# Optimization experiments

Measured on AMD Instinct MI355X. Metric: run time of the kernel, lower is better.

The kernel has to match this reference:

```python
import jax, jax.numpy as jnp
import numpy as np

EPS = 1e-5

def conv1x1(x, W, b):
    # x: [B,Cin,H,W], W: [Cout,Cin], b: [Cout]
    return jnp.einsum('bchw,oc->bohw', x, W) + b[None, :, None, None]

def mean_variance_norm(feat):
    # feat: [B,C,H,W]; torch .var(dim=2) is unbiased (ddof=1)
    B, C, H, W = feat.shape
    flat = feat.reshape(B, C, H * W)
    mean = flat.mean(axis=2)[:, :, None, None]
    std = jnp.sqrt(flat.var(axis=2, ddof=1) + EPS)[:, :, None, None]
    return (feat - mean) / std

def setup_inputs() -> dict:
    key = jax.random.key(0)
    ks = jax.random.split(key, 10)
    B, C, H, W = 4, 512, 64, 64
    sc = 0.02
    return {
        'content': jax.random.normal(ks[0], (B, C, H, W), jnp.float32),
        'style': jax.random.normal(ks[1], (B, C, H, W), jnp.float32),
        'content_key': jax.random.normal(ks[2], (B, C, H, W), jnp.float32),
        'style_key': jax.random.normal(ks[3], (B, C, H, W), jnp.float32),
        'Wf': jax.random.normal(ks[4], (C, C), jnp.float32) * sc,
        'bf': jax.random.normal(ks[5], (C,), jnp.float32) * sc,
        'Wg': jax.random.normal(ks[6], (C, C), jnp.float32) * sc,
        'bg': jax.random.normal(ks[7], (C,), jnp.float32) * sc,
        'Wh': jax.random.normal(ks[8], (C, C), jnp.float32) * sc,
        'bh': jax.random.normal(ks[9], (C,), jnp.float32) * sc,
    }

def reference(content, style, content_key, style_key, Wf, bf, Wg, bg, Wh, bh):
    B, C, H, W = content.shape
    F = conv1x1(content_key, Wf, bf)          # [B,Ck,H,W]
    G = conv1x1(style_key, Wg, bg)            # [B,Ck,Hs,Ws]
    Hv = conv1x1(style, Wh, bh)               # [B,C,Hs,Ws]
    Ck = F.shape[1]
    N = H * W
    M = G.shape[2] * G.shape[3]
    Fq = F.reshape(B, Ck, N).transpose(0, 2, 1)        # [B,N,Ck]
    Gk = G.reshape(B, Ck, M)                            # [B,Ck,M]
    style_flat = Hv.reshape(B, C, M).transpose(0, 2, 1)  # [B,M,C]
    S = jax.nn.softmax(jnp.einsum('bnc,bcm->bnm', Fq, Gk), axis=-1)  # [B,N,M]
    mean = jnp.einsum('bnm,bmc->bnc', S, style_flat)                  # [B,N,C]
    second = jnp.einsum('bnm,bmc->bnc', S, style_flat ** 2)
    std = jnp.sqrt(jax.nn.relu(second - mean ** 2))
    mean = mean.reshape(B, H, W, C).transpose(0, 3, 1, 2)
    std = std.reshape(B, H, W, C).transpose(0, 3, 1, 2)
    return std * mean_variance_norm(content) + mean
```

## Files before the change

kernel.cpp:

```cpp
#include <hip/hip_runtime.h>

#define B_ 4
#define C_ 512
#define N_ 4096

typedef unsigned short u16;
typedef _Float16 f16;
typedef f16 f16x8 __attribute__((ext_vector_type(8)));
typedef float f32x4 __attribute__((ext_vector_type(4)));

#define MFMA16(a, b, c) __builtin_amdgcn_mfma_f32_16x16x32_f16(a, b, c, 0, 0, 0)

__device__ __forceinline__ u16 f2h(float f) {
  union { f16 h; u16 u; } x; x.h = (f16)f; return x.u;
}
__device__ __forceinline__ float h2f(u16 v) {
  union { u16 u; f16 h; } x; x.u = v; return (float)x.h;
}
__device__ __forceinline__ f16x8 ldA(const void* p) {
  union { uint4 u; f16x8 v; } x; x.u = *(const uint4*)p; return x.v;
}

__global__ __launch_bounds__(256) void cast_w_kernel(const float* __restrict__ in,
                                                     u16* __restrict__ out, int n) {
  int i = (blockIdx.x * 256 + threadIdx.x) * 4;
  if (i >= n) return;
  float4 v = *(const float4*)(in + i);
  uint2 p;
  p.x = f2h(v.x) | ((unsigned)f2h(v.y) << 16);
  p.y = f2h(v.z) | ((unsigned)f2h(v.w) << 16);
  *(uint2*)(out + i) = p;
}

__global__ __launch_bounds__(256) void transpose_cast_kernel(const float* __restrict__ in,
                                                             u16* __restrict__ out) {
  __shared__ float ld[64][65];
  const int b = blockIdx.z, n0 = blockIdx.x * 64, c0 = blockIdx.y * 64;
  const int t = threadIdx.x;
  {
    const int r = t >> 2, q4 = (t & 3) * 16;
    const float* ip = in + ((size_t)(b * C_ + c0 + r)) * N_ + n0 + q4;
#pragma unroll
    for (int j = 0; j < 4; ++j) {
      float4 v = *(const float4*)(ip + j * 4);
      ld[r][q4 + j * 4 + 0] = v.x; ld[r][q4 + j * 4 + 1] = v.y;
      ld[r][q4 + j * 4 + 2] = v.z; ld[r][q4 + j * 4 + 3] = v.w;
    }
  }
  __syncthreads();
  {
    const int r2 = t >> 2, c16 = (t & 3) * 16;
    unsigned pk[8];
#pragma unroll
    for (int j = 0; j < 8; ++j) {
      unsigned lo = f2h(ld[c16 + j * 2 + 0][r2]);
      unsigned hi = f2h(ld[c16 + j * 2 + 1][r2]);
      pk[j] = lo | (hi << 16);
    }
    u16* op = out + ((size_t)(b * N_ + n0 + r2)) * C_ + c0 + c16;
    *(uint4*)(op + 0) = make_uint4(pk[0], pk[1], pk[2], pk[3]);
    *(uint4*)(op + 8) = make_uint4(pk[4], pk[5], pk[6], pk[7]);
  }
}

__global__ __launch_bounds__(512, 4) void conv_kernel(const u16* __restrict__ Xt,
                                                      const u16* __restrict__ Wb,
                                                      const float* __restrict__ bias,
                                                      u16* __restrict__ Outp,
                                                      u16* __restrict__ OutT) {
  __shared__ char sm[65536];
  const int b = blockIdx.z, n0 = blockIdx.x * 64, o0 = blockIdx.y * 64;
  const int t = threadIdx.x, w = t >> 6, lane = t & 63;
  const int wr = w >> 1, wc = w & 1, l15 = lane & 15, l4 = lane >> 4;
#pragma unroll
  for (int k = 0; k < 8; ++k) {
    int ch = t + k * 512, row = ch >> 6, c16 = ch & 63;
    uint4 xv = *(const uint4*)(Xt + ((size_t)(b * N_ + n0 + row)) * C_ + c16 * 8);
    *(uint4*)(sm + row * 1024 + ((c16 ^ (row & 7)) << 4)) = xv;
  }
  __syncthreads();
  f32x4 acc0 = {0, 0, 0, 0}, acc1 = {0, 0, 0, 0};
  const int arow = wr * 16 + l15;
  const int oA = o0 + wc * 32 + l15, oB = oA + 16;
  const u16* wp0 = Wb + (size_t)oA * C_ + l4 * 8;
  const u16* wp1 = Wb + (size_t)oB * C_ + l4 * 8;
#pragma unroll
  for (int kf = 0; kf < 16; ++kf) {
    f16x8 a = ldA(sm + arow * 1024 + (((kf * 4 + l4) ^ (arow & 7)) << 4));
    f16x8 w0 = ldA(wp0 + kf * 32);
    f16x8 w1 = ldA(wp1 + kf * 32);
    acc0 = MFMA16(a, w0, acc0);
    acc1 = MFMA16(a, w1, acc1);
  }
  const float b0 = bias[oA], b1 = bias[oB];
  if (OutT == nullptr) {
#pragma unroll
    for (int r = 0; r < 4; ++r) {
      int n = n0 + wr * 16 + l4 * 4 + r;
      size_t base = ((size_t)(b * N_ + n)) * C_;
      Outp[base + oA] = f2h(acc0[r] + b0);
      Outp[base + oB] = f2h(acc1[r] + b1);
    }
  } else {
    __syncthreads();
    u16* ldsT = (u16*)sm;
#pragma unroll
    for (int r = 0; r < 4; ++r) {
      int nl = wr * 16 + l4 * 4 + r;
      ldsT[(oA - o0) * 72 + nl] = f2h(acc0[r] + b0);
      ldsT[(oB - o0) * 72 + nl] = f2h(acc1[r] + b1);
    }
    __syncthreads();
    const int orow = t >> 3, n8 = (t & 7) * 8;
    uint4 v = *(const uint4*)&ldsT[orow * 72 + n8];
    *(uint4*)(OutT + ((size_t)(b * C_ + o0 + orow)) * N_ + n0 + n8) = v;
  }
}

#define LQ  0
#define LG  65536
#define LV  98304
#define LP  139264
#define LF  144384
#define LL  144640

__global__ __launch_bounds__(1024, 4) void attn_dual_kernel(const u16* __restrict__ Ft,
                                                            const u16* __restrict__ Gt,
                                                            const u16* __restrict__ V,
                                                            float* __restrict__ OutM,
                                                            float* __restrict__ OutS) {
  __shared__ char sm[144896];
  char* ldsQ = sm + LQ; char* ldsG = sm + LG; char* ldsV = sm + LV; char* ldsP = sm + LP;
  float* facv = (float*)(sm + LF);
  float* lbuf = (float*)(sm + LL);

  const int b = blockIdx.y, n0 = blockIdx.x * 64;
  const int t = threadIdx.x, w = t >> 6, lane = t & 63;
  const int l15 = lane & 15, l4 = lane >> 4;
  const int ri = w >> 2, ci = w & 3;

#pragma unroll
  for (int k = 0; k < 4; ++k) {
    int ch = t + k * 1024, row = ch >> 6, c16 = ch & 63;
    uint4 qv = *(const uint4*)(Ft + ((size_t)(b * N_ + n0 + row)) * C_ + c16 * 8);
    *(uint4*)(ldsQ + row * 1024 + ((c16 ^ (row & 7)) << 4)) = qv;
  }
#pragma unroll
  for (int k = 0; k < 2; ++k) {
    int ch = t + k * 1024, row = ch >> 6, c16 = ch & 63;
    uint4 gv = *(const uint4*)(Gt + ((size_t)(b * N_ + row)) * C_ + c16 * 8);
    *(uint4*)(ldsG + row * 1024 + ((c16 ^ (row & 7)) << 4)) = gv;
  }

  f32x4 accM[8], accS[8];
#pragma unroll
  for (int i = 0; i < 8; ++i) { accM[i] = (f32x4){0,0,0,0}; accS[i] = (f32x4){0,0,0,0}; }
  float m_run[4] = {-1e30f, -1e30f, -1e30f, -1e30f};
  float l_run[4] = {0, 0, 0, 0};

  const u16* Vb = V + (size_t)(b * C_) * N_;
  __syncthreads();

  for (int it = 0; it < 128; ++it) {
    const int m0 = it * 32;

    if (w < 4) {
      f32x4 s0 = {0, 0, 0, 0}, s1 = {0, 0, 0, 0};
      {
        const int qrow = w * 16 + l15;
        const int g0r = l15, g1r = 16 + l15;
#pragma unroll
        for (int kf = 0; kf < 16; ++kf) {
          int c16 = kf * 4 + l4;
          f16x8 qf = ldA(ldsQ + qrow * 1024 + ((c16 ^ (qrow & 7)) << 4));
          f16x8 ga = ldA(ldsG + g0r * 1024 + ((c16 ^ (g0r & 7)) << 4));
          f16x8 gb = ldA(ldsG + g1r * 1024 + ((c16 ^ (g1r & 7)) << 4));
          s0 = MFMA16(qf, ga, s0);
          s1 = MFMA16(qf, gb, s1);
        }
      }
      float rmax[4];
#pragma unroll
      for (int r = 0; r < 4; ++r) rmax[r] = fmaxf(s0[r], s1[r]);
#pragma unroll
      for (int off = 1; off < 16; off <<= 1)
#pragma unroll
        for (int r = 0; r < 4; ++r) rmax[r] = fmaxf(rmax[r], __shfl_xor(rmax[r], off));
      float fac0[4], rsum[4];
#pragma unroll
      for (int r = 0; r < 4; ++r) {
        float mn = fmaxf(m_run[r], rmax[r]);
        fac0[r] = __expf(m_run[r] - mn);
        float p0 = __expf(s0[r] - mn);
        float p1 = __expf(s1[r] - mn);
        u16 pb0 = f2h(p0), pb1 = f2h(p1);
        rsum[r] = h2f(pb0) + h2f(pb1);
        int row = w * 16 + l4 * 4 + r;
        *(u16*)(ldsP + row * 80 + l15 * 2) = pb0;
        *(u16*)(ldsP + row * 80 + 32 + l15 * 2) = pb1;
        m_run[r] = mn;
      }
#pragma unroll
      for (int off = 1; off < 16; off <<= 1)
#pragma unroll
        for (int r = 0; r < 4; ++r) rsum[r] += __shfl_xor(rsum[r], off);
      if (l15 == 0)
#pragma unroll
        for (int r = 0; r < 4; ++r) {
          int row = w * 16 + l4 * 4 + r;
          l_run[r] = l_run[r] * fac0[r] + rsum[r];
          facv[row] = fac0[r];
        }
      else
#pragma unroll
        for (int r = 0; r < 4; ++r) l_run[r] = l_run[r] * fac0[r] + rsum[r];
    } else if (w < 12) {
      const int t2 = t - 256;
#pragma unroll
      for (int k = 0; k < 4; ++k) {
        int ch = t2 + k * 512, c = ch >> 2, sl = ch & 3;
        uint4 vv = *(const uint4*)(Vb + (size_t)c * N_ + m0 + sl * 8);
        *(uint4*)(ldsV + c * 80 + sl * 16) = vv;
      }
    }
    __syncthreads();

    if (w >= 12 && it < 127) {
      const int t3 = t - 768;
      const u16* gb_ = Gt + ((size_t)(b * N_ + m0 + 32)) * C_;
#pragma unroll
      for (int k = 0; k < 8; ++k) {
        int ch = t3 + k * 256, row = ch >> 6, c16 = ch & 63;
        uint4 gv = *(const uint4*)(gb_ + (size_t)row * C_ + c16 * 8);
        *(uint4*)(ldsG + row * 1024 + ((c16 ^ (row & 7)) << 4)) = gv;
      }
    }
    float fr[4];
#pragma unroll
    for (int r = 0; r < 4; ++r) fr[r] = facv[ri * 16 + l4 * 4 + r];
    bool nch = true;
#pragma unroll
    for (int r = 0; r < 4; ++r) nch = nch && (fr[r] == 1.0f);
    if (!__all(nch)) {
#pragma unroll
      for (int f = 0; f < 8; ++f)
#pragma unroll
        for (int r = 0; r < 4; ++r) { accM[f][r] *= fr[r]; accS[f][r] *= fr[r]; }
    }
    {
      const int arow = ri * 16 + l15;
      f16x8 a = ldA(ldsP + arow * 80 + l4 * 16);
#pragma unroll
      for (int f = 0; f < 8; ++f) {
        const int c = ci * 128 + f * 16 + l15;
        f16x8 v0 = ldA(ldsV + c * 80 + l4 * 16);
        accM[f] = MFMA16(a, v0, accM[f]);
        f16x8 w0 = v0 * v0;
        accS[f] = MFMA16(a, w0, accS[f]);
      }
    }
    __syncthreads();
  }

  if (w < 4 && l15 == 0)
#pragma unroll
    for (int r = 0; r < 4; ++r) lbuf[w * 16 + l4 * 4 + r] = l_run[r];
  __syncthreads();
  float rl[4];
#pragma unroll
  for (int r = 0; r < 4; ++r) rl[r] = 1.0f / lbuf[ri * 16 + l4 * 4 + r];
#pragma unroll
  for (int f = 0; f < 8; ++f) {
    const int c = ci * 128 + f * 16 + l15;
#pragma unroll
    for (int r = 0; r < 4; ++r) {
      int n = n0 + ri * 16 + l4 * 4 + r;
      size_t o = ((size_t)(b * N_ + n)) * C_ + c;
      OutM[o] = accM[f][r] * rl[r];
      OutS[o] = accS[f][r] * rl[r];
    }
  }
}

__global__ __launch_bounds__(256) void stats_kernel(const float* __restrict__ content,
                                                    float* __restrict__ stats) {
  const int c = blockIdx.x, b = blockIdx.y;
  const float4* p = (const float4*)(content + ((size_t)(b * C_ + c)) * N_);
  float s = 0.f, ss = 0.f;
  for (int i = threadIdx.x; i < N_ / 4; i += 256) {
    float4 v = p[i];
    s += v.x + v.y + v.z + v.w;
    ss += v.x * v.x + v.y * v.y + v.z * v.z + v.w * v.w;
  }
#pragma unroll
  for (int off = 32; off; off >>= 1) { s += __shfl_down(s, off); ss += __shfl_down(ss, off); }
  __shared__ float as_[4], ass_[4];
  int w = threadIdx.x >> 6;
  if ((threadIdx.x & 63) == 0) { as_[w] = s; ass_[w] = ss; }
  __syncthreads();
  if (threadIdx.x == 0) {
    float S = as_[0] + as_[1] + as_[2] + as_[3];
    float SS = ass_[0] + ass_[1] + ass_[2] + ass_[3];
    float mu = S * (1.0f / N_);
    float var = (SS - (float)N_ * mu * mu) * (1.0f / (N_ - 1));
    stats[(size_t)(b * C_ + c) * 2 + 0] = mu;
    stats[(size_t)(b * C_ + c) * 2 + 1] = rsqrtf(var + 1e-5f);
  }
}

__global__ __launch_bounds__(256) void combine_kernel(const float* __restrict__ content,
                                                      const float* __restrict__ meanb,
                                                      const float* __restrict__ secb,
                                                      const float* __restrict__ stats,
                                                      float* __restrict__ outp) {
  __shared__ float ldM[64][65], ldS[64][65];
  const int b = blockIdx.z, n0 = blockIdx.x * 64, c0 = blockIdx.y * 64;
  const int t = threadIdx.x;
  {
    const int r = t >> 2, q4 = (t & 3) * 16;
    size_t ib = ((size_t)(b * N_ + n0 + r)) * C_ + c0 + q4;
#pragma unroll
    for (int j = 0; j < 4; ++j) {
      float4 mv = *(const float4*)(meanb + ib + j * 4);
      float4 sv = *(const float4*)(secb + ib + j * 4);
      ldM[r][q4 + j * 4 + 0] = mv.x; ldM[r][q4 + j * 4 + 1] = mv.y;
      ldM[r][q4 + j * 4 + 2] = mv.z; ldM[r][q4 + j * 4 + 3] = mv.w;
      ldS[r][q4 + j * 4 + 0] = sv.x; ldS[r][q4 + j * 4 + 1] = sv.y;
      ldS[r][q4 + j * 4 + 2] = sv.z; ldS[r][q4 + j * 4 + 3] = sv.w;
    }
  }
  __syncthreads();
  const int n4 = (t & 15) * 4, cb = t >> 4;
#pragma unroll
  for (int cc = 0; cc < 4; ++cc) {
    int c_loc = cc * 16 + cb;
    int c = c0 + c_loc;
    float mu = stats[(size_t)(b * C_ + c) * 2 + 0];
    float rs = stats[(size_t)(b * C_ + c) * 2 + 1];
    size_t gb = ((size_t)(b * C_ + c)) * N_ + n0 + n4;
    float4 xv = *(const float4*)(content + gb);
    float4 ov;
    {
      float m0_ = ldM[n4 + 0][c_loc], s0_ = ldS[n4 + 0][c_loc];
      float m1_ = ldM[n4 + 1][c_loc], s1_ = ldS[n4 + 1][c_loc];
      float m2_ = ldM[n4 + 2][c_loc], s2_ = ldS[n4 + 2][c_loc];
      float m3_ = ldM[n4 + 3][c_loc], s3_ = ldS[n4 + 3][c_loc];
      ov.x = sqrtf(fmaxf(s0_ - m0_ * m0_, 0.f)) * ((xv.x - mu) * rs) + m0_;
      ov.y = sqrtf(fmaxf(s1_ - m1_ * m1_, 0.f)) * ((xv.y - mu) * rs) + m1_;
      ov.z = sqrtf(fmaxf(s2_ - m2_ * m2_, 0.f)) * ((xv.z - mu) * rs) + m2_;
      ov.w = sqrtf(fmaxf(s3_ - m3_ * m3_, 0.f)) * ((xv.w - mu) * rs) + m3_;
    }
    *(float4*)(outp + gb) = ov;
  }
}

extern "C" void kernel_launch(void* const* d_in, const int* in_sizes, int n_in,
                              void* d_out, int out_size, void* d_ws, size_t ws_size,
                              hipStream_t stream) {
  (void)in_sizes; (void)n_in; (void)out_size; (void)ws_size;
  const float* content = (const float*)d_in[0];
  const float* style   = (const float*)d_in[1];
  const float* ckey    = (const float*)d_in[2];
  const float* skey    = (const float*)d_in[3];
  const float* Wf = (const float*)d_in[4]; const float* bf_ = (const float*)d_in[5];
  const float* Wg = (const float*)d_in[6]; const float* bg_ = (const float*)d_in[7];
  const float* Wh = (const float*)d_in[8]; const float* bh_ = (const float*)d_in[9];
  float* outp = (float*)d_out;
  char* ws = (char*)d_ws;

  const size_t MB = 1u << 20;
  u16*   Ft    = (u16*)(ws + 0 * MB);
  u16*   Gt    = (u16*)(ws + 16 * MB);
  u16*   Hv    = (u16*)(ws + 32 * MB);
  float* stats = (float*)(ws + 48 * MB);
  u16*   Xt    = (u16*)(ws + 48 * MB);
  float* meanb = (float*)(ws + 64 * MB);
  float* secb  = (float*)(ws + 96 * MB);
  u16*   Wb3   = (u16*)(ws + 80 * MB);
  u16* Wbf = Wb3, *Wbg = Wb3 + 262144, *Wbh = Wb3 + 524288;

  const dim3 gT(64, 8, 4);

  cast_w_kernel<<<256, 256, 0, stream>>>(Wf, Wbf, 262144);
  cast_w_kernel<<<256, 256, 0, stream>>>(Wg, Wbg, 262144);
  cast_w_kernel<<<256, 256, 0, stream>>>(Wh, Wbh, 262144);

  transpose_cast_kernel<<<gT, 256, 0, stream>>>(ckey, Xt);
  conv_kernel<<<gT, 512, 0, stream>>>(Xt, Wbf, bf_, Ft, nullptr);
  transpose_cast_kernel<<<gT, 256, 0, stream>>>(skey, Xt);
  conv_kernel<<<gT, 512, 0, stream>>>(Xt, Wbg, bg_, Gt, nullptr);
  transpose_cast_kernel<<<gT, 256, 0, stream>>>(style, Xt);
  conv_kernel<<<gT, 512, 0, stream>>>(Xt, Wbh, bh_, nullptr, Hv);

  stats_kernel<<<dim3(C_, B_), 256, 0, stream>>>(content, stats);
  attn_dual_kernel<<<dim3(64, B_), 1024, 0, stream>>>(Ft, Gt, Hv, meanb, secb);
  combine_kernel<<<gT, 256, 0, stream>>>(content, meanb, secb, stats, outp);
}
```

Measured before the change: 894.3 us.

## Fuse transpose-cast into 1x1 conv kernel, computing all output channels per block

Replaces the separate transpose/cast-to-fp16 pass plus conv kernel with one kernel that loads fp32 input tiles, transposes and casts them through LDS into a swizzled fp16 tile, then loops over all 512 output channels. This removes the intermediate Xt buffer round-trip through global memory and the extra launches per conv. The trade-off is a grid of only 256 blocks, each doing eight times the work serially with larger LDS use (about 80KB), which may lower occupancy and parallelism on a large GPU.

```diff
diff --git a/kernel.cpp b/kernel.cpp
--- a/kernel.cpp
+++ b/kernel.cpp
@@ -32,88 +32,84 @@
   *(uint2*)(out + i) = p;
 }
 
-__global__ __launch_bounds__(256) void transpose_cast_kernel(const float* __restrict__ in,
-                                                             u16* __restrict__ out) {
-  __shared__ float ld[64][65];
-  const int b = blockIdx.z, n0 = blockIdx.x * 64, c0 = blockIdx.y * 64;
-  const int t = threadIdx.x;
-  {
-    const int r = t >> 2, q4 = (t & 3) * 16;
-    const float* ip = in + ((size_t)(b * C_ + c0 + r)) * N_ + n0 + q4;
-#pragma unroll
-    for (int j = 0; j < 4; ++j) {
-      float4 v = *(const float4*)(ip + j * 4);
-      ld[r][q4 + j * 4 + 0] = v.x; ld[r][q4 + j * 4 + 1] = v.y;
-      ld[r][q4 + j * 4 + 2] = v.z; ld[r][q4 + j * 4 + 3] = v.w;
-    }
-  }
-  __syncthreads();
-  {
-    const int r2 = t >> 2, c16 = (t & 3) * 16;
-    unsigned pk[8];
-#pragma unroll
-    for (int j = 0; j < 8; ++j) {
-      unsigned lo = f2h(ld[c16 + j * 2 + 0][r2]);
-      unsigned hi = f2h(ld[c16 + j * 2 + 1][r2]);
-      pk[j] = lo | (hi << 16);
-    }
-    u16* op = out + ((size_t)(b * N_ + n0 + r2)) * C_ + c0 + c16;
-    *(uint4*)(op + 0) = make_uint4(pk[0], pk[1], pk[2], pk[3]);
-    *(uint4*)(op + 8) = make_uint4(pk[4], pk[5], pk[6], pk[7]);
-  }
-}
-
-__global__ __launch_bounds__(512, 4) void conv_kernel(const u16* __restrict__ Xt,
-                                                      const u16* __restrict__ Wb,
-                                                      const float* __restrict__ bias,
-                                                      u16* __restrict__ Outp,
-                                                      u16* __restrict__ OutT) {
-  __shared__ char sm[65536];
-  const int b = blockIdx.z, n0 = blockIdx.x * 64, o0 = blockIdx.y * 64;
+#define FCA 0
+#define FCB 65536
+
+__global__ __launch_bounds__(512, 4) void conv_fused_kernel(const float* __restrict__ X,
+                                                            const u16* __restrict__ Wb,
+                                                            const float* __restrict__ bias,
+                                                            u16* __restrict__ Outp,
+                                                            u16* __restrict__ OutT) {
+  __shared__ char sm[82176];
+  float* ld = (float*)(sm + FCB);
+  const int b = blockIdx.y, n0 = blockIdx.x * 64;
   const int t = threadIdx.x, w = t >> 6, lane = t & 63;
   const int wr = w >> 1, wc = w & 1, l15 = lane & 15, l4 = lane >> 4;
-#pragma unroll
-  for (int k = 0; k < 8; ++k) {
-    int ch = t + k * 512, row = ch >> 6, c16 = ch & 63;
-    uint4 xv = *(const uint4*)(Xt + ((size_t)(b * N_ + n0 + row)) * C_ + c16 * 8);
-    *(uint4*)(sm + row * 1024 + ((c16 ^ (row & 7)) << 4)) = xv;
-  }
-  __syncthreads();
-  f32x4 acc0 = {0, 0, 0, 0}, acc1 = {0, 0, 0, 0};
-  const int arow = wr * 16 + l15;
-  const int oA = o0 + wc * 32 + l15, oB = oA + 16;
-  const u16* wp0 = Wb + (size_t)oA * C_ + l4 * 8;
-  const u16* wp1 = Wb + (size_t)oB * C_ + l4 * 8;
-#pragma unroll
-  for (int kf = 0; kf < 16; ++kf) {
-    f16x8 a = ldA(sm + arow * 1024 + (((kf * 4 + l4) ^ (arow & 7)) << 4));
-    f16x8 w0 = ldA(wp0 + kf * 32);
-    f16x8 w1 = ldA(wp1 + kf * 32);
-    acc0 = MFMA16(a, w0, acc0);
-    acc1 = MFMA16(a, w1, acc1);
-  }
-  const float b0 = bias[oA], b1 = bias[oB];
-  if (OutT == nullptr) {
-#pragma unroll
-    for (int r = 0; r < 4; ++r) {
-      int n = n0 + wr * 16 + l4 * 4 + r;
-      size_t base = ((size_t)(b * N_ + n)) * C_;
-      Outp[base + oA] = f2h(acc0[r] + b0);
-      Outp[base + oB] = f2h(acc1[r] + b1);
-    }
-  } else {
+
+  for (int cc = 0; cc < 8; ++cc) {
+    {
+      const int r = t >> 3, q8 = (t & 7) * 8;
+      const float* ip = X + ((size_t)(b * C_ + cc * 64 + r)) * N_ + n0 + q8;
+      float4 v0 = *(const float4*)(ip);
+      float4 v1 = *(const float4*)(ip + 4);
+      float* lr = ld + r * 65 + q8;
+      lr[0] = v0.x; lr[1] = v0.y; lr[2] = v0.z; lr[3] = v0.w;
+      lr[4] = v1.x; lr[5] = v1.y; lr[6] = v1.z; lr[7] = v1.w;
+    }
     __syncthreads();
-    u16* ldsT = (u16*)sm;
-#pragma unroll
-    for (int r = 0; r < 4; ++r) {
-      int nl = wr * 16 + l4 * 4 + r;
-      ldsT[(oA - o0) * 72 + nl] = f2h(acc0[r] + b0);
-      ldsT[(oB - o0) * 72 + nl] = f2h(acc1[r] + b1);
+    {
+      const int r2 = t >> 3, c8 = (t & 7) * 8;
+      unsigned pk[4];
+#pragma unroll
+      for (int j = 0; j < 4; ++j) {
+        unsigned lo = f2h(ld[(c8 + j * 2 + 0) * 65 + r2]);
+        unsigned hi = f2h(ld[(c8 + j * 2 + 1) * 65 + r2]);
+        pk[j] = lo | (hi << 16);
+      }
+      const int c16 = cc * 8 + (t & 7);
+      *(uint4*)(sm + r2 * 1024 + ((c16 ^ (r2 & 7)) << 4)) =
+          make_uint4(pk[0], pk[1], pk[2], pk[3]);
     }
     __syncthreads();
-    const int orow = t >> 3, n8 = (t & 7) * 8;
-    uint4 v = *(const uint4*)&ldsT[orow * 72 + n8];
-    *(uint4*)(OutT + ((size_t)(b * C_ + o0 + orow)) * N_ + n0 + n8) = v;
+  }
+
+  for (int o0 = 0; o0 < 512; o0 += 64) {
+    f32x4 acc0 = {0, 0, 0, 0}, acc1 = {0, 0, 0, 0};
+    const int arow = wr * 16 + l15;
+    const int oA = o0 + wc * 32 + l15, oB = oA + 16;
+    const u16* wp0 = Wb + (size_t)oA * C_ + l4 * 8;
+    const u16* wp1 = Wb + (size_t)oB * C_ + l4 * 8;
+#pragma unroll
+    for (int kf = 0; kf < 16; ++kf) {
+      f16x8 a = ldA(sm + arow * 1024 + (((kf * 4 + l4) ^ (arow & 7)) << 4));
+      f16x8 w0 = ldA(wp0 + kf * 32);
+      f16x8 w1 = ldA(wp1 + kf * 32);
+      acc0 = MFMA16(a, w0, acc0);
+      acc1 = MFMA16(a, w1, acc1);
+    }
+    const float b0 = bias[oA], b1 = bias[oB];
+    if (OutT == nullptr) {
+#pragma unroll
+      for (int r = 0; r < 4; ++r) {
+        int n = n0 + wr * 16 + l4 * 4 + r;
+        size_t base = ((size_t)(b * N_ + n)) * C_;
+        Outp[base + oA] = f2h(acc0[r] + b0);
+        Outp[base + oB] = f2h(acc1[r] + b1);
+      }
+    } else {
+      u16* ldsT = (u16*)(sm + FCB);
+#pragma unroll
+      for (int r = 0; r < 4; ++r) {
+        int nl = wr * 16 + l4 * 4 + r;
+        ldsT[(oA - o0) * 72 + nl] = f2h(acc0[r] + b0);
+        ldsT[(oB - o0) * 72 + nl] = f2h(acc1[r] + b1);
+      }
+      __syncthreads();
+      const int orow = t >> 3, n8 = (t & 7) * 8;
+      uint4 v = *(const uint4*)&ldsT[orow * 72 + n8];
+      *(uint4*)(OutT + ((size_t)(b * C_ + o0 + orow)) * N_ + n0 + n8) = v;
+      __syncthreads();
+    }
   }
 }
 
@@ -373,24 +369,21 @@
   u16*   Gt    = (u16*)(ws + 16 * MB);
   u16*   Hv    = (u16*)(ws + 32 * MB);
   float* stats = (float*)(ws + 48 * MB);
-  u16*   Xt    = (u16*)(ws + 48 * MB);
   float* meanb = (float*)(ws + 64 * MB);
   float* secb  = (float*)(ws + 96 * MB);
   u16*   Wb3   = (u16*)(ws + 80 * MB);
   u16* Wbf = Wb3, *Wbg = Wb3 + 262144, *Wbh = Wb3 + 524288;
 
   const dim3 gT(64, 8, 4);
+  const dim3 gC(64, B_);
 
   cast_w_kernel<<<256, 256, 0, stream>>>(Wf, Wbf, 262144);
   cast_w_kernel<<<256, 256, 0, stream>>>(Wg, Wbg, 262144);
   cast_w_kernel<<<256, 256, 0, stream>>>(Wh, Wbh, 262144);
 
-  transpose_cast_kernel<<<gT, 256, 0, stream>>>(ckey, Xt);
-  conv_kernel<<<gT, 512, 0, stream>>>(Xt, Wbf, bf_, Ft, nullptr);
-  transpose_cast_kernel<<<gT, 256, 0, stream>>>(skey, Xt);
-  conv_kernel<<<gT, 512, 0, stream>>>(Xt, Wbg, bg_, Gt, nullptr);
-  transpose_cast_kernel<<<gT, 256, 0, stream>>>(style, Xt);
-  conv_kernel<<<gT, 512, 0, stream>>>(Xt, Wbh, bh_, nullptr, Hv);
+  conv_fused_kernel<<<gC, 512, 0, stream>>>(ckey, Wbf, bf_, Ft, nullptr);
+  conv_fused_kernel<<<gC, 512, 0, stream>>>(skey, Wbg, bg_, Gt, nullptr);
+  conv_fused_kernel<<<gC, 512, 0, stream>>>(style, Wbh, bh_, nullptr, Hv);
 
   stats_kernel<<<dim3(C_, B_), 256, 0, stream>>>(content, stats);
   attn_dual_kernel<<<dim3(64, B_), 1024, 0, stream>>>(Ft, Gt, Hv, meanb, secb);
```

Result: faster. 874.5 us (-2.2%).
